# Kernel tuning notes

Measured on AMD Instinct MI355X. Metric: run time of the kernel, lower is better.

Reference implementation:

```python
import jax, jax.numpy as jnp
import numpy as np

N_NODES = 50000
N_EDGES = 800000
D = 128
EPS = 1e-5


def _glorot(key, shape):
    fan_in, fan_out = shape[0], shape[1] if len(shape) > 1 else 1
    s = jnp.sqrt(2.0 / (fan_in + fan_out))
    return jax.random.normal(key, shape, dtype=jnp.float32) * s


def setup_inputs() -> dict:
    key = jax.random.key(0)
    ks = jax.random.split(key, 16)
    h = jax.random.normal(ks[0], (N_NODES, D), dtype=jnp.float32)
    e = jax.random.normal(ks[1], (N_EDGES, D), dtype=jnp.float32)
    src = jax.random.randint(ks[2], (N_EDGES,), 0, N_NODES, dtype=jnp.int32)
    dst = jax.random.randint(ks[3], (N_EDGES,), 0, N_NODES, dtype=jnp.int32)
    # weights stored [in, out] (i.e. torch W.T); biases [out]
    W_fc = _glorot(ks[4], (D, D))
    W_fce = _glorot(ks[5], (D, D))
    a_attn = _glorot(ks[6], (3 * D,))      # attn_fc weight (out=1)
    a_attn_e = _glorot(ks[7], (3 * D,))    # attn_fc_e weight
    W_B1 = _glorot(ks[8], (D, D)); b_B1 = jnp.zeros((D,), jnp.float32)
    W_B2 = _glorot(ks[9], (D, D)); b_B2 = jnp.zeros((D,), jnp.float32)
    W_B3 = _glorot(ks[10], (D, D)); b_B3 = jnp.zeros((D,), jnp.float32)
    W_mix = _glorot(ks[11], (2 * D, D)); b_mix = jnp.zeros((D,), jnp.float32)
    ln_g = jnp.ones((D,), jnp.float32); ln_b = jnp.zeros((D,), jnp.float32)
    return dict(h=h, e=e, src=src, dst=dst, W_fc=W_fc, W_fce=W_fce,
                a_attn=a_attn, a_attn_e=a_attn_e,
                W_B1=W_B1, b_B1=b_B1, W_B2=W_B2, b_B2=b_B2,
                W_B3=W_B3, b_B3=b_B3, W_mix=W_mix, b_mix=b_mix,
                ln_g=ln_g, ln_b=ln_b)


def _segment_softmax(scores, seg, num_segments):
    # scores: [E]; softmax over edges sharing the same destination node
    m = jax.ops.segment_max(scores, seg, num_segments=num_segments)
    ex = jnp.exp(scores - m[seg])
    denom = jax.ops.segment_sum(ex, seg, num_segments=num_segments)
    return ex / denom[seg]


def _gat_side(z, z_e, s, d_idx, a_attn, a_attn_e, W_mix, b_mix, n):
    # attn_fc(concat[z_src, z_e, z_dst]) split into three small matvecs
    d = z.shape[1]
    zs1, zs2, zs3 = z @ a_attn[:d], z_e @ a_attn[d:2 * d], z @ a_attn[2 * d:]
    ze1, ze2, ze3 = z @ a_attn_e[:d], z_e @ a_attn_e[d:2 * d], z @ a_attn_e[2 * d:]
    score = jax.nn.leaky_relu(zs1[s] + zs2 + zs3[d_idx], negative_slope=0.01)
    score_e = jax.nn.leaky_relu(ze1[s] + ze2 + ze3[d_idx], negative_slope=0.01)
    alpha = _segment_softmax(score, d_idx, n)
    alpha_e = _segment_softmax(score_e, d_idx, n)
    h_agg = jax.ops.segment_sum(alpha[:, None] * z[s], d_idx, num_segments=n)
    he_agg = jax.ops.segment_sum(alpha_e[:, None] * z_e, d_idx, num_segments=n)
    return jnp.concatenate([h_agg, he_agg], axis=-1) @ W_mix + b_mix


def reference(h, e, src, dst, W_fc, W_fce, a_attn, a_attn_e,
              W_B1, b_B1, W_B2, b_B2, W_B3, b_B3, W_mix, b_mix, ln_g, ln_b):
    n = h.shape[0]
    B1h = h @ W_B1 + b_B1
    B2h = h @ W_B2 + b_B2
    B3e = e @ W_B3 + b_B3
    # forward-graph edge update: e_ji = relu(B1h[u] + B2h[v] + B3e) + e (residual)
    e_ji = jax.nn.relu(B1h[src] + B2h[dst] + B3e) + e
    z = h @ W_fc
    z_e = e_ji @ W_fce
    # forward graph aggregates into dst; reverse graph into src
    h_f = _gat_side(z, z_e, src, dst, a_attn, a_attn_e, W_mix, b_mix, n)
    h_r = _gat_side(z, z_e, dst, src, a_attn, a_attn_e, W_mix, b_mix, n)
    h_out = h_f + h_r
    # LayerNorm (batch_norm=False branch)
    mu = jnp.mean(h_out, axis=-1, keepdims=True)
    var = jnp.var(h_out, axis=-1, keepdims=True)
    h_out = (h_out - mu) / jnp.sqrt(var + EPS) * ln_g + ln_b
    h_out = jax.nn.relu(h_out) + h  # residual; dropout=0 (eval)
    return h_out, e_ji
```

## Files before the change

### kernel.cpp

```cpp
#include <hip/hip_runtime.h>
#include <hip/hip_bf16.h>


typedef _Float16 f16x8 __attribute__((ext_vector_type(8)));
typedef _Float16 f16x4 __attribute__((ext_vector_type(4)));
typedef _Float16 f16x2 __attribute__((ext_vector_type(2)));
typedef float f32x4 __attribute__((ext_vector_type(4)));

__device__ inline float lrelu(float x) { return x > 0.f ? x : 0.01f * x; }

__device__ inline unsigned short f2bf(float f) {
  unsigned u = __float_as_uint(f);
  unsigned r = (u + 0x7FFFu + ((u >> 16) & 1u)) >> 16;
  return (unsigned short)r;
}
__device__ inline float bf2f(unsigned short us) {
  return __uint_as_float(((unsigned)us) << 16);
}

__global__ void k_combine(const float* __restrict__ Wfc, const float* __restrict__ Wfce,
                          const float* __restrict__ Wmix, const float* __restrict__ aat,
                          const float* __restrict__ aate, _Float16* __restrict__ McT,
                          float* __restrict__ cvec) {
  int b = blockIdx.x, j = threadIdx.x;
  if (b < 256) {
    const float* Arow;
    const float* Wm;
    if (b < 128) { Arow = Wfc + b * 128; Wm = Wmix; }
    else         { Arow = Wfce + (b - 128) * 128; Wm = Wmix + 128 * 128; }
    float acc = 0.f;
    for (int t = 0; t < 128; ++t) acc += Arow[t] * Wm[t * 128 + j];
    McT[j * 256 + b] = (_Float16)acc;
  } else {
    int idx = b - 256;
    const float* W; const float* a;
    switch (idx) {
      case 0: W = Wfc;  a = aat;        break;
      case 1: W = Wfce; a = aat + 128;  break;
      case 2: W = Wfc;  a = aat + 256;  break;
      case 3: W = Wfc;  a = aate;       break;
      case 4: W = Wfce; a = aate + 128; break;
      default: W = Wfc; a = aate + 256; break;
    }
    float acc = 0.f;
    for (int t = 0; t < 128; ++t) acc += W[j * 128 + t] * a[t];
    cvec[idx * 128 + j] = acc;
  }
}

__global__ __launch_bounds__(256) void k_wt3(const float* __restrict__ W3,
                                             const float* __restrict__ W1,
                                             const float* __restrict__ W2,
                                             _Float16* __restrict__ WT,
                                             _Float16* __restrict__ W1T,
                                             _Float16* __restrict__ W2T) {
  int idx = blockIdx.x * 256 + threadIdx.x;
  int which = idx >> 14;
  int r = idx & 16383;
  int c = r >> 7, k = r & 127;
  const float* s = (which == 0) ? W3 : (which == 1) ? W1 : W2;
  _Float16* d = (which == 0) ? WT : (which == 1) ? W1T : W2T;
  d[r] = (_Float16)s[k * 128 + c];
}

__global__ __launch_bounds__(256) void k_gemm_dual(const float* __restrict__ A,
                                                   const _Float16* __restrict__ W1T,
                                                   const float* __restrict__ b1v,
                                                   const _Float16* __restrict__ W2T,
                                                   const float* __restrict__ b2v,
                                                   const float* __restrict__ cvec,
                                                   unsigned short* __restrict__ B1hh,
                                                   unsigned short* __restrict__ B2hh,
                                                   unsigned short* __restrict__ hh,
                                                   float* __restrict__ zs1, float* __restrict__ zs3,
                                                   float* __restrict__ ze1, float* __restrict__ ze3,
                                                   int M) {
  __shared__ float Als[64][132];
  int tid = threadIdx.x;
  int lane = tid & 63, w = tid >> 6;
  int kgrp = lane >> 4, sub = lane & 15;
  long mbase = (long)blockIdx.x * 64;
#pragma unroll
  for (int it = 0; it < 8; ++it) {
    int idx = tid + it * 256;
    int r = idx >> 5, cv = idx & 31;
    long m = mbase + r;
    float4 v = make_float4(0.f, 0.f, 0.f, 0.f);
    if (m < M) v = *(const float4*)&A[m * 128 + 4 * cv];
    *(float4*)&Als[r][4 * cv] = v;
  }
  __syncthreads();

  int arow = w * 16 + sub;
  f16x8 afr[4];
#pragma unroll
  for (int ks = 0; ks < 4; ++ks) {
    float4 u0 = *(const float4*)&Als[arow][ks * 32 + kgrp * 8];
    float4 u1 = *(const float4*)&Als[arow][ks * 32 + kgrp * 8 + 4];
    f16x8 a;
    a[0] = (_Float16)u0.x; a[1] = (_Float16)u0.y; a[2] = (_Float16)u0.z; a[3] = (_Float16)u0.w;
    a[4] = (_Float16)u1.x; a[5] = (_Float16)u1.y; a[6] = (_Float16)u1.z; a[7] = (_Float16)u1.w;
    afr[ks] = a;
  }

  f32x4 acc1[8], acc2[8];
#pragma unroll
  for (int t = 0; t < 8; ++t) {
    acc1[t] = (f32x4){0.f, 0.f, 0.f, 0.f};
    acc2[t] = (f32x4){0.f, 0.f, 0.f, 0.f};
  }
#pragma unroll
  for (int ks = 0; ks < 4; ++ks)
#pragma unroll
    for (int t = 0; t < 8; ++t) {
      int boff = (t * 16 + sub) * 128 + ks * 32 + kgrp * 8;
      f16x8 b1 = *(const f16x8*)&W1T[boff];
      acc1[t] = __builtin_amdgcn_mfma_f32_16x16x32_f16(afr[ks], b1, acc1[t], 0, 0, 0);
      f16x8 b2 = *(const f16x8*)&W2T[boff];
      acc2[t] = __builtin_amdgcn_mfma_f32_16x16x32_f16(afr[ks], b2, acc2[t], 0, 0, 0);
    }

  float bb1[8], bb2[8];
#pragma unroll
  for (int t = 0; t < 8; ++t) {
    int c = t * 16 + sub;
    bb1[t] = b1v[c];
    bb2[t] = b2v[c];
  }

#pragma unroll
  for (int r = 0; r < 4; ++r) {
    int rl = w * 16 + kgrp * 4 + r;
    long m = mbase + rl;
    float p1 = 0.f, p3 = 0.f, q1 = 0.f, q3 = 0.f;
    if (m < M) {
#pragma unroll
      for (int t = 0; t < 8; ++t) {
        int c = t * 16 + sub;
        float a = Als[rl][c];
        B1hh[m * 128 + c] = f2bf(acc1[t][r] + bb1[t]);
        B2hh[m * 128 + c] = f2bf(acc2[t][r] + bb2[t]);
        hh[m * 128 + c] = f2bf(a);
        p1 += a * cvec[c];
        p3 += a * cvec[256 + c];
        q1 += a * cvec[384 + c];
        q3 += a * cvec[640 + c];
      }
    }
#pragma unroll
    for (int mk = 1; mk < 16; mk <<= 1) {
      p1 += __shfl_xor(p1, mk); p3 += __shfl_xor(p3, mk);
      q1 += __shfl_xor(q1, mk); q3 += __shfl_xor(q3, mk);
    }
    if (m < M && sub == 0) { zs1[m] = p1; zs3[m] = p3; ze1[m] = q1; ze3[m] = q3; }
  }
}

__global__ __launch_bounds__(256) void k_edge(const float* __restrict__ e,
                                              const _Float16* __restrict__ WT,
                                              const float* __restrict__ bias,
                                              const unsigned short* __restrict__ B1hh,
                                              const unsigned short* __restrict__ B2hh,
                                              const int* __restrict__ src, const int* __restrict__ dst,
                                              const float* __restrict__ cs2, const float* __restrict__ ce2,
                                              float* __restrict__ eout, unsigned short* __restrict__ ejh,
                                              float* __restrict__ zs2, float* __restrict__ ze2, int M) {
  __shared__ _Float16 Els[64][136];
  int tid = threadIdx.x;
  int lane = tid & 63, w = tid >> 6;
  int kgrp = lane >> 4, sub = lane & 15;
  long mbase = (long)blockIdx.x * 64;
#pragma unroll
  for (int it = 0; it < 8; ++it) {
    int idx = tid + it * 256;
    int r = idx >> 5, cv = idx & 31;
    long m = mbase + r;
    float4 v = make_float4(0.f, 0.f, 0.f, 0.f);
    if (m < M) v = *(const float4*)&e[m * 128 + 4 * cv];
    f16x4 hv;
    hv[0] = (_Float16)v.x; hv[1] = (_Float16)v.y;
    hv[2] = (_Float16)v.z; hv[3] = (_Float16)v.w;
    *(f16x4*)&Els[r][4 * cv] = hv;
  }
  __syncthreads();

  int arow = w * 16 + sub;
  f16x8 afr[4];
#pragma unroll
  for (int ks = 0; ks < 4; ++ks)
    afr[ks] = *(const f16x8*)&Els[arow][ks * 32 + kgrp * 8];

  f32x4 acc[8];
#pragma unroll
  for (int t = 0; t < 8; ++t) acc[t] = (f32x4){0.f, 0.f, 0.f, 0.f};
#pragma unroll
  for (int ks = 0; ks < 4; ++ks)
#pragma unroll
    for (int t = 0; t < 8; ++t) {
      f16x8 b = *(const f16x8*)&WT[(t * 16 + sub) * 128 + ks * 32 + kgrp * 8];
      acc[t] = __builtin_amdgcn_mfma_f32_16x16x32_f16(afr[ks], b, acc[t], 0, 0, 0);
    }

  float bb[8], cs[8], ce[8];
#pragma unroll
  for (int t = 0; t < 8; ++t) {
    int c = t * 16 + sub;
    bb[t] = bias[c];
    cs[t] = cs2[c];
    ce[t] = ce2[c];
  }

#pragma unroll
  for (int r = 0; r < 4; ++r) {
    int rl = w * 16 + kgrp * 4 + r;
    long m = mbase + rl;
    float ps = 0.f, pe = 0.f;
    if (m < M) {
      int s = src[m], dv = dst[m];
      const unsigned short* b1p = B1hh + (long)s * 128;
      const unsigned short* b2p = B2hh + (long)dv * 128;
#pragma unroll
      for (int t = 0; t < 8; ++t) {
        int c = t * 16 + sub;
        float o = fmaxf(acc[t][r] + bb[t] + bf2f(b1p[c]) + bf2f(b2p[c]), 0.f) + (float)Els[rl][c];
        eout[m * 128 + c] = o;
        ejh[m * 128 + c] = f2bf(o);
        ps += o * cs[t];
        pe += o * ce[t];
      }
    }
#pragma unroll
    for (int mk = 1; mk < 16; mk <<= 1) {
      ps += __shfl_xor(ps, mk);
      pe += __shfl_xor(pe, mk);
    }
    if (m < M && sub == 0) { zs2[m] = ps; ze2[m] = pe; }
  }
}

__global__ void k_hist(const int* __restrict__ src, const int* __restrict__ dst,
                       int* __restrict__ cntf, int* __restrict__ cntr, int E) {
  int e = blockIdx.x * 256 + threadIdx.x;
  if (e < E) {
    atomicAdd(&cntf[dst[e]], 1);
    atomicAdd(&cntr[src[e]], 1);
  }
}

__global__ __launch_bounds__(1024) void k_scan(const int* __restrict__ cntf,
                                               const int* __restrict__ cntr,
                                               int* __restrict__ offf, int* __restrict__ offr, int n) {
  __shared__ int part[1024];
  int tid = threadIdx.x;
  for (int pass = 0; pass < 2; ++pass) {
    const int* cnt = pass ? cntr : cntf;
    int* off = pass ? offr : offf;
    int per = (n + 1023) >> 10;
    int beg = tid * per; if (beg > n) beg = n;
    int end = beg + per; if (end > n) end = n;
    int s = 0;
    for (int i = beg; i < end; ++i) s += cnt[i];
    part[tid] = s;
    __syncthreads();
    for (int o = 1; o < 1024; o <<= 1) {
      int vv = (tid >= o) ? part[tid - o] : 0;
      __syncthreads();
      part[tid] += vv;
      __syncthreads();
    }
    int run = tid ? part[tid - 1] : 0;
    for (int i = beg; i < end; ++i) { off[i] = run; run += cnt[i]; }
    if (tid == 1023) off[n] = part[1023];
    __syncthreads();
  }
}

__global__ void k_fill(const int* __restrict__ src, const int* __restrict__ dst,
                       const int* __restrict__ offf, const int* __restrict__ offr,
                       int* __restrict__ curf, int* __restrict__ curr,
                       int* __restrict__ eidf, int* __restrict__ eidr, int E) {
  int e = blockIdx.x * 256 + threadIdx.x;
  if (e >= E) return;
  int d = dst[e];
  int p = atomicAdd(&curf[d], 1);
  eidf[offf[d] + p] = e;
  int s = src[e];
  p = atomicAdd(&curr[s], 1);
  eidr[offr[s] + p] = e;
}

__global__ void k_scores(const int* __restrict__ src, const int* __restrict__ dst,
                         const int* __restrict__ eidf, const int* __restrict__ eidr,
                         const float* __restrict__ zs1, const float* __restrict__ zs2,
                         const float* __restrict__ zs3, const float* __restrict__ ze1,
                         const float* __restrict__ ze2, const float* __restrict__ ze3,
                         float* __restrict__ sf, float* __restrict__ sef,
                         float* __restrict__ sr, float* __restrict__ ser, int E) {
  int p = blockIdx.x * 256 + threadIdx.x;
  if (p >= E) return;
  {
    int e = eidf[p];
    int s = src[e], d = dst[e];
    float z2 = zs2[e], ze2v = ze2[e];
    sf[p] = lrelu(zs1[s] + z2 + zs3[d]);
    sef[p] = lrelu(ze1[s] + ze2v + ze3[d]);
  }
  {
    int e = eidr[p];
    int s = src[e], d = dst[e];
    float z2 = zs2[e], ze2v = ze2[e];
    sr[p] = lrelu(zs1[d] + z2 + zs3[s]);
    ser[p] = lrelu(ze1[d] + ze2v + ze3[s]);
  }
}

__device__ inline float wred_max64(float v) {
#pragma unroll
  for (int mk = 32; mk; mk >>= 1) v = fmaxf(v, __shfl_xor(v, mk));
  return v;
}
__device__ inline float wred_sum64(float v) {
#pragma unroll
  for (int mk = 32; mk; mk >>= 1) v += __shfl_xor(v, mk);
  return v;
}

__global__ __launch_bounds__(256) void k_agg4(const int* __restrict__ offf, const int* __restrict__ eidf,
                                              const int* __restrict__ offr, const int* __restrict__ eidr,
                                              const int* __restrict__ src, const int* __restrict__ dst,
                                              const float* __restrict__ sf, const float* __restrict__ sef,
                                              const float* __restrict__ sr, const float* __restrict__ ser,
                                              const unsigned short* __restrict__ hh,
                                              const unsigned short* __restrict__ ejh,
                                              _Float16* __restrict__ agg2, int n) {
  int gw = blockIdx.x * 4 + (threadIdx.x >> 6);
  int lane = threadIdx.x & 63;
  if (gw >= 2 * n) return;
  int dir = gw & 1;
  int v = gw >> 1;
  const int* off = dir ? offr : offf;
  const int* eid = dir ? eidr : eidf;
  const float* sc  = dir ? sr  : sf;
  const float* sce = dir ? ser : sef;
  const int* nbr = dir ? dst : src;
  int s0 = off[v], s1 = off[v + 1];
  float m1 = -1e30f, m2 = -1e30f;
  for (int i = s0 + lane; i < s1; i += 64) {
    m1 = fmaxf(m1, sc[i]);
    m2 = fmaxf(m2, sce[i]);
  }
  m1 = wred_max64(m1); m2 = wred_max64(m2);
  float d1 = 0.f, d2 = 0.f;
  for (int i = s0 + lane; i < s1; i += 64) {
    d1 += __expf(sc[i] - m1);
    d2 += __expf(sce[i] - m2);
  }
  d1 = wred_sum64(d1); d2 = wred_sum64(d2);
  float i1 = (s1 > s0) ? 1.f / d1 : 0.f;
  float i2 = (s1 > s0) ? 1.f / d2 : 0.f;
  float aH0 = 0.f, aH1 = 0.f, aE0 = 0.f, aE1 = 0.f;
  int i = s0;
  for (; i + 3 < s1; i += 4) {
    int eA = eid[i], eB = eid[i + 1], eC = eid[i + 2], eD = eid[i + 3];
    int nA = nbr[eA], nB = nbr[eB], nC = nbr[eC], nD = nbr[eD];
    unsigned hpA = *(const unsigned*)&hh[(long)nA * 128 + 2 * lane];
    unsigned epA = *(const unsigned*)&ejh[(long)eA * 128 + 2 * lane];
    unsigned hpB = *(const unsigned*)&hh[(long)nB * 128 + 2 * lane];
    unsigned epB = *(const unsigned*)&ejh[(long)eB * 128 + 2 * lane];
    unsigned hpC = *(const unsigned*)&hh[(long)nC * 128 + 2 * lane];
    unsigned epC = *(const unsigned*)&ejh[(long)eC * 128 + 2 * lane];
    unsigned hpD = *(const unsigned*)&hh[(long)nD * 128 + 2 * lane];
    unsigned epD = *(const unsigned*)&ejh[(long)eD * 128 + 2 * lane];
    float w1A = __expf(sc[i] - m1) * i1,     w2A = __expf(sce[i] - m2) * i2;
    float w1B = __expf(sc[i + 1] - m1) * i1, w2B = __expf(sce[i + 1] - m2) * i2;
    float w1C = __expf(sc[i + 2] - m1) * i1, w2C = __expf(sce[i + 2] - m2) * i2;
    float w1D = __expf(sc[i + 3] - m1) * i1, w2D = __expf(sce[i + 3] - m2) * i2;
    aH0 += w1A * bf2f((unsigned short)(hpA & 0xFFFFu)) + w1B * bf2f((unsigned short)(hpB & 0xFFFFu))
         + w1C * bf2f((unsigned short)(hpC & 0xFFFFu)) + w1D * bf2f((unsigned short)(hpD & 0xFFFFu));
    aH1 += w1A * bf2f((unsigned short)(hpA >> 16)) + w1B * bf2f((unsigned short)(hpB >> 16))
         + w1C * bf2f((unsigned short)(hpC >> 16)) + w1D * bf2f((unsigned short)(hpD >> 16));
    aE0 += w2A * bf2f((unsigned short)(epA & 0xFFFFu)) + w2B * bf2f((unsigned short)(epB & 0xFFFFu))
         + w2C * bf2f((unsigned short)(epC & 0xFFFFu)) + w2D * bf2f((unsigned short)(epD & 0xFFFFu));
    aE1 += w2A * bf2f((unsigned short)(epA >> 16)) + w2B * bf2f((unsigned short)(epB >> 16))
         + w2C * bf2f((unsigned short)(epC >> 16)) + w2D * bf2f((unsigned short)(epD >> 16));
  }
  for (; i < s1; ++i) {
    int e_ = eid[i];
    int nb = nbr[e_];
    float w1 = __expf(sc[i] - m1) * i1;
    float w2 = __expf(sce[i] - m2) * i2;
    unsigned hp = *(const unsigned*)&hh[(long)nb * 128 + 2 * lane];
    unsigned ep = *(const unsigned*)&ejh[(long)e_ * 128 + 2 * lane];
    aH0 += w1 * bf2f((unsigned short)(hp & 0xFFFFu));
    aH1 += w1 * bf2f((unsigned short)(hp >> 16));
    aE0 += w2 * bf2f((unsigned short)(ep & 0xFFFFu));
    aE1 += w2 * bf2f((unsigned short)(ep >> 16));
  }
  _Float16* dstp = agg2 + ((long)dir * n + v) * 256;
  *(f16x2*)&dstp[2 * lane] = (f16x2){(_Float16)aH0, (_Float16)aH1};
  *(f16x2*)&dstp[128 + 2 * lane] = (f16x2){(_Float16)aE0, (_Float16)aE1};
}

__global__ __launch_bounds__(256) void k_mix_ln(const _Float16* __restrict__ A,
                                                const _Float16* __restrict__ McT,
                                                const float* __restrict__ bias,
                                                const float* __restrict__ h,
                                                const float* __restrict__ g,
                                                const float* __restrict__ bn,
                                                float* __restrict__ outp, int M) {
  __shared__ _Float16 Als[64][264];
  int tid = threadIdx.x;
  int lane = tid & 63, w = tid >> 6;
  int kgrp = lane >> 4, sub = lane & 15;
  long mbase = (long)blockIdx.x * 64;
  const _Float16* A2 = A + (long)M * 256;
#pragma unroll
  for (int it = 0; it < 8; ++it) {
    int idx = tid + it * 256;
    int r = idx >> 5, c8 = (idx & 31) * 8;
    long m = mbase + r;
    f16x8 hv = (f16x8){0, 0, 0, 0, 0, 0, 0, 0};
    if (m < M) {
      f16x8 v1 = *(const f16x8*)&A[m * 256 + c8];
      f16x8 v2 = *(const f16x8*)&A2[m * 256 + c8];
#pragma unroll
      for (int j = 0; j < 8; ++j) hv[j] = (_Float16)((float)v1[j] + (float)v2[j]);
    }
    *(f16x8*)&Als[r][c8] = hv;
  }
  __syncthreads();

  int arow = w * 16 + sub;
  f32x4 acc[8];
#pragma unroll
  for (int t = 0; t < 8; ++t) acc[t] = (f32x4){0.f, 0.f, 0.f, 0.f};
#pragma unroll
  for (int ks = 0; ks < 8; ++ks) {
    f16x8 a = *(const f16x8*)&Als[arow][ks * 32 + kgrp * 8];
#pragma unroll
    for (int t = 0; t < 8; ++t) {
      f16x8 b = *(const f16x8*)&McT[(t * 16 + sub) * 256 + ks * 32 + kgrp * 8];
      acc[t] = __builtin_amdgcn_mfma_f32_16x16x32_f16(a, b, acc[t], 0, 0, 0);
    }
  }

  float bb[8], gv[8], bv[8];
#pragma unroll
  for (int t = 0; t < 8; ++t) {
    int c = t * 16 + sub;
    bb[t] = 2.f * bias[c];
    gv[t] = g[c];
    bv[t] = bn[c];
  }

#pragma unroll
  for (int r = 0; r < 4; ++r) {
    int rl = w * 16 + kgrp * 4 + r;
    long m = mbase + rl;
    float x[8];
    float s = 0.f, q = 0.f;
#pragma unroll
    for (int t = 0; t < 8; ++t) {
      x[t] = acc[t][r] + bb[t];
      s += x[t];
      q += x[t] * x[t];
    }
#pragma unroll
    for (int mk = 1; mk < 16; mk <<= 1) {
      s += __shfl_xor(s, mk);
      q += __shfl_xor(q, mk);
    }
    float mu = s * (1.f / 128.f);
    float var = q * (1.f / 128.f) - mu * mu;
    float rstd = rsqrtf(var + 1e-5f);
    if (m < M) {
      const float* hp = h + m * 128;
#pragma unroll
      for (int t = 0; t < 8; ++t) {
        int c = t * 16 + sub;
        outp[m * 128 + c] = fmaxf((x[t] - mu) * rstd * gv[t] + bv[t], 0.f) + hp[c];
      }
    }
  }
}

extern "C" void kernel_launch(void* const* d_in, const int* in_sizes, int n_in,
                              void* d_out, int out_size, void* d_ws, size_t ws_size,
                              hipStream_t stream) {
  const float* h = (const float*)d_in[0];
  const float* e = (const float*)d_in[1];
  const int* src = (const int*)d_in[2];
  const int* dst = (const int*)d_in[3];
  const float* Wfc = (const float*)d_in[4];
  const float* Wfce = (const float*)d_in[5];
  const float* aat = (const float*)d_in[6];
  const float* aate = (const float*)d_in[7];
  const float* WB1 = (const float*)d_in[8];
  const float* bB1 = (const float*)d_in[9];
  const float* WB2 = (const float*)d_in[10];
  const float* bB2 = (const float*)d_in[11];
  const float* WB3 = (const float*)d_in[12];
  const float* bB3 = (const float*)d_in[13];
  const float* Wmix = (const float*)d_in[14];
  const float* bmix = (const float*)d_in[15];
  const float* lng = (const float*)d_in[16];
  const float* lnb = (const float*)d_in[17];
  int n = in_sizes[0] / 128;
  int E = in_sizes[1] / 128;

  float* hout = (float*)d_out;
  float* eout = (float*)d_out + (size_t)n * 128;

  char* w = (char*)d_ws;
  auto alloc = [&](size_t bytes) {
    void* p = w;
    w += (bytes + 255) / 256 * 256;
    return p;
  };
  unsigned short* B1hh = (unsigned short*)alloc((size_t)n * 128 * 2);
  unsigned short* B2hh = (unsigned short*)alloc((size_t)n * 128 * 2);
  _Float16* agg2 = (_Float16*)alloc((size_t)n * 512 * 2);
  float* zs1 = (float*)alloc((size_t)n * 4);
  float* zs3 = (float*)alloc((size_t)n * 4);
  float* ze1 = (float*)alloc((size_t)n * 4);
  float* ze3 = (float*)alloc((size_t)n * 4);
  float* zs2 = (float*)alloc((size_t)E * 4);
  float* ze2 = (float*)alloc((size_t)E * 4);
  float* sf = (float*)alloc((size_t)E * 4);
  float* sef = (float*)alloc((size_t)E * 4);
  float* sr = (float*)alloc((size_t)E * 4);
  float* ser = (float*)alloc((size_t)E * 4);
  float* cvec = (float*)alloc(768 * 4);
  _Float16* WT = (_Float16*)alloc(128 * 128 * 2);
  _Float16* W1T = (_Float16*)alloc(128 * 128 * 2);
  _Float16* W2T = (_Float16*)alloc(128 * 128 * 2);
  _Float16* McT = (_Float16*)alloc(128 * 256 * 2);
  int* offf = (int*)alloc((size_t)(n + 1) * 4);
  int* offr = (int*)alloc((size_t)(n + 1) * 4);
  size_t curpad = ((size_t)n * 4 + 255) / 256 * 256;
  int* curf = (int*)alloc((size_t)n * 4);
  int* curr = (int*)alloc((size_t)n * 4);
  int* eidf = (int*)alloc((size_t)E * 4);
  int* eidr = (int*)alloc((size_t)E * 4);
  unsigned short* ejh = (unsigned short*)alloc((size_t)E * 128 * 2);
  unsigned short* hh = (unsigned short*)alloc((size_t)n * 128 * 2);

  hipMemsetAsync(curf, 0, curpad * 2, stream);

  k_combine<<<262, 128, 0, stream>>>(Wfc, Wfce, Wmix, aat, aate, McT, cvec);
  k_wt3<<<192, 256, 0, stream>>>(WB3, WB1, WB2, WT, W1T, W2T);
  k_gemm_dual<<<(n + 63) / 64, 256, 0, stream>>>(h, W1T, bB1, W2T, bB2, cvec, B1hh, B2hh, hh,
                                                 zs1, zs3, ze1, ze3, n);
  k_hist<<<(E + 255) / 256, 256, 0, stream>>>(src, dst, curf, curr, E);
  k_scan<<<1, 1024, 0, stream>>>(curf, curr, offf, offr, n);
  hipMemsetAsync(curf, 0, curpad * 2, stream);
  k_fill<<<(E + 255) / 256, 256, 0, stream>>>(src, dst, offf, offr, curf, curr, eidf, eidr, E);
  k_edge<<<(E + 63) / 64, 256, 0, stream>>>(e, WT, bB3, B1hh, B2hh, src, dst,
                                            cvec + 128, cvec + 512, eout, ejh, zs2, ze2, E);
  k_scores<<<(E + 255) / 256, 256, 0, stream>>>(src, dst, eidf, eidr, zs1, zs2, zs3, ze1, ze2, ze3,
                                                sf, sef, sr, ser, E);
  k_agg4<<<(2 * n + 3) / 4, 256, 0, stream>>>(offf, eidf, offr, eidr, src, dst, sf, sef, sr, ser,
                                              hh, ejh, agg2, n);
  k_mix_ln<<<(n + 63) / 64, 256, 0, stream>>>(agg2, McT, bmix, h, lng, lnb, hout, n);
}
```

Baseline: 1.080 ms.

## Store bf16 edge features in forward-CSR order and precompute neighbor indices

k_edge now writes the bf16 copy of e_ji at each edge's forward-CSR position (posf), so the forward aggregation reads edge rows contiguously instead of gathering them through eidf. k_scores also materialises per-slot neighbor ids (nf, nr) and reverse-direction row positions (er2), which removes the double-indirection eid->src/dst lookups from k_agg4. The cost is scattered bf16 writes in k_edge, extra index arrays and writes in k_fill and k_scores, and a branch in k_agg4 that duplicates its loop per direction.

```diff
diff --git a/kernel.cpp b/kernel.cpp
--- a/kernel.cpp
+++ b/kernel.cpp
@@ -162,6 +162,7 @@
                                               const unsigned short* __restrict__ B1hh,
                                               const unsigned short* __restrict__ B2hh,
                                               const int* __restrict__ src, const int* __restrict__ dst,
+                                              const int* __restrict__ posf,
                                               const float* __restrict__ cs2, const float* __restrict__ ce2,
                                               float* __restrict__ eout, unsigned short* __restrict__ ejh,
                                               float* __restrict__ zs2, float* __restrict__ ze2, int M) {
@@ -217,6 +218,7 @@
     float ps = 0.f, pe = 0.f;
     if (m < M) {
       int s = src[m], dv = dst[m];
+      long pf = posf[m];
       const unsigned short* b1p = B1hh + (long)s * 128;
       const unsigned short* b2p = B2hh + (long)dv * 128;
 #pragma unroll
@@ -224,7 +226,7 @@
         int c = t * 16 + sub;
         float o = fmaxf(acc[t][r] + bb[t] + bf2f(b1p[c]) + bf2f(b2p[c]), 0.f) + (float)Els[rl][c];
         eout[m * 128 + c] = o;
-        ejh[m * 128 + c] = f2bf(o);
+        ejh[pf * 128 + c] = f2bf(o);
         ps += o * cs[t];
         pe += o * ce[t];
       }
@@ -278,12 +280,15 @@
 __global__ void k_fill(const int* __restrict__ src, const int* __restrict__ dst,
                        const int* __restrict__ offf, const int* __restrict__ offr,
                        int* __restrict__ curf, int* __restrict__ curr,
-                       int* __restrict__ eidf, int* __restrict__ eidr, int E) {
+                       int* __restrict__ eidf, int* __restrict__ eidr,
+                       int* __restrict__ posf, int* E_unused, int E) {
   int e = blockIdx.x * 256 + threadIdx.x;
   if (e >= E) return;
   int d = dst[e];
   int p = atomicAdd(&curf[d], 1);
-  eidf[offf[d] + p] = e;
+  int qf = offf[d] + p;
+  eidf[qf] = e;
+  posf[e] = qf;
   int s = src[e];
   p = atomicAdd(&curr[s], 1);
   eidr[offr[s] + p] = e;
@@ -291,11 +296,14 @@
 
 __global__ void k_scores(const int* __restrict__ src, const int* __restrict__ dst,
                          const int* __restrict__ eidf, const int* __restrict__ eidr,
+                         const int* __restrict__ posf,
                          const float* __restrict__ zs1, const float* __restrict__ zs2,
                          const float* __restrict__ zs3, const float* __restrict__ ze1,
                          const float* __restrict__ ze2, const float* __restrict__ ze3,
                          float* __restrict__ sf, float* __restrict__ sef,
-                         float* __restrict__ sr, float* __restrict__ ser, int E) {
+                         float* __restrict__ sr, float* __restrict__ ser,
+                         int* __restrict__ nf, int* __restrict__ nr,
+                         int* __restrict__ er2, int E) {
   int p = blockIdx.x * 256 + threadIdx.x;
   if (p >= E) return;
   {
@@ -304,6 +312,7 @@
     float z2 = zs2[e], ze2v = ze2[e];
     sf[p] = lrelu(zs1[s] + z2 + zs3[d]);
     sef[p] = lrelu(ze1[s] + ze2v + ze3[d]);
+    nf[p] = s;
   }
   {
     int e = eidr[p];
@@ -311,6 +320,8 @@
     float z2 = zs2[e], ze2v = ze2[e];
     sr[p] = lrelu(zs1[d] + z2 + zs3[s]);
     ser[p] = lrelu(ze1[d] + ze2v + ze3[s]);
+    nr[p] = d;
+    er2[p] = posf[e];
   }
 }
 
@@ -325,9 +336,10 @@
   return v;
 }
 
-__global__ __launch_bounds__(256) void k_agg4(const int* __restrict__ offf, const int* __restrict__ eidf,
-                                              const int* __restrict__ offr, const int* __restrict__ eidr,
-                                              const int* __restrict__ src, const int* __restrict__ dst,
+__global__ __launch_bounds__(256) void k_agg4(const int* __restrict__ offf,
+                                              const int* __restrict__ offr,
+                                              const int* __restrict__ nf, const int* __restrict__ nr,
+                                              const int* __restrict__ er2,
                                               const float* __restrict__ sf, const float* __restrict__ sef,
                                               const float* __restrict__ sr, const float* __restrict__ ser,
                                               const unsigned short* __restrict__ hh,
@@ -339,10 +351,9 @@
   int dir = gw & 1;
   int v = gw >> 1;
   const int* off = dir ? offr : offf;
-  const int* eid = dir ? eidr : eidf;
   const float* sc  = dir ? sr  : sf;
   const float* sce = dir ? ser : sef;
-  const int* nbr = dir ? dst : src;
+  const int* nbArr = dir ? nr : nf;
   int s0 = off[v], s1 = off[v + 1];
   float m1 = -1e30f, m2 = -1e30f;
   for (int i = s0 + lane; i < s1; i += 64) {
@@ -360,41 +371,78 @@
   float i2 = (s1 > s0) ? 1.f / d2 : 0.f;
   float aH0 = 0.f, aH1 = 0.f, aE0 = 0.f, aE1 = 0.f;
   int i = s0;
-  for (; i + 3 < s1; i += 4) {
-    int eA = eid[i], eB = eid[i + 1], eC = eid[i + 2], eD = eid[i + 3];
-    int nA = nbr[eA], nB = nbr[eB], nC = nbr[eC], nD = nbr[eD];
-    unsigned hpA = *(const unsigned*)&hh[(long)nA * 128 + 2 * lane];
-    unsigned epA = *(const unsigned*)&ejh[(long)eA * 128 + 2 * lane];
-    unsigned hpB = *(const unsigned*)&hh[(long)nB * 128 + 2 * lane];
-    unsigned epB = *(const unsigned*)&ejh[(long)eB * 128 + 2 * lane];
-    unsigned hpC = *(const unsigned*)&hh[(long)nC * 128 + 2 * lane];
-    unsigned epC = *(const unsigned*)&ejh[(long)eC * 128 + 2 * lane];
-    unsigned hpD = *(const unsigned*)&hh[(long)nD * 128 + 2 * lane];
-    unsigned epD = *(const unsigned*)&ejh[(long)eD * 128 + 2 * lane];
-    float w1A = __expf(sc[i] - m1) * i1,     w2A = __expf(sce[i] - m2) * i2;
-    float w1B = __expf(sc[i + 1] - m1) * i1, w2B = __expf(sce[i + 1] - m2) * i2;
-    float w1C = __expf(sc[i + 2] - m1) * i1, w2C = __expf(sce[i + 2] - m2) * i2;
-    float w1D = __expf(sc[i + 3] - m1) * i1, w2D = __expf(sce[i + 3] - m2) * i2;
-    aH0 += w1A * bf2f((unsigned short)(hpA & 0xFFFFu)) + w1B * bf2f((unsigned short)(hpB & 0xFFFFu))
-         + w1C * bf2f((unsigned short)(hpC & 0xFFFFu)) + w1D * bf2f((unsigned short)(hpD & 0xFFFFu));
-    aH1 += w1A * bf2f((unsigned short)(hpA >> 16)) + w1B * bf2f((unsigned short)(hpB >> 16))
-         + w1C * bf2f((unsigned short)(hpC >> 16)) + w1D * bf2f((unsigned short)(hpD >> 16));
-    aE0 += w2A * bf2f((unsigned short)(epA & 0xFFFFu)) + w2B * bf2f((unsigned short)(epB & 0xFFFFu))
-         + w2C * bf2f((unsigned short)(epC & 0xFFFFu)) + w2D * bf2f((unsigned short)(epD & 0xFFFFu));
-    aE1 += w2A * bf2f((unsigned short)(epA >> 16)) + w2B * bf2f((unsigned short)(epB >> 16))
-         + w2C * bf2f((unsigned short)(epC >> 16)) + w2D * bf2f((unsigned short)(epD >> 16));
-  }
-  for (; i < s1; ++i) {
-    int e_ = eid[i];
-    int nb = nbr[e_];
-    float w1 = __expf(sc[i] - m1) * i1;
-    float w2 = __expf(sce[i] - m2) * i2;
-    unsigned hp = *(const unsigned*)&hh[(long)nb * 128 + 2 * lane];
-    unsigned ep = *(const unsigned*)&ejh[(long)e_ * 128 + 2 * lane];
-    aH0 += w1 * bf2f((unsigned short)(hp & 0xFFFFu));
-    aH1 += w1 * bf2f((unsigned short)(hp >> 16));
-    aE0 += w2 * bf2f((unsigned short)(ep & 0xFFFFu));
-    aE1 += w2 * bf2f((unsigned short)(ep >> 16));
+  if (dir == 0) {
+    for (; i + 3 < s1; i += 4) {
+      int nA = nf[i], nB = nf[i + 1], nC = nf[i + 2], nD = nf[i + 3];
+      unsigned hpA = *(const unsigned*)&hh[(long)nA * 128 + 2 * lane];
+      unsigned epA = *(const unsigned*)&ejh[(long)i * 128 + 2 * lane];
+      unsigned hpB = *(const unsigned*)&hh[(long)nB * 128 + 2 * lane];
+      unsigned epB = *(const unsigned*)&ejh[(long)(i + 1) * 128 + 2 * lane];
+      unsigned hpC = *(const unsigned*)&hh[(long)nC * 128 + 2 * lane];
+      unsigned epC = *(const unsigned*)&ejh[(long)(i + 2) * 128 + 2 * lane];
+      unsigned hpD = *(const unsigned*)&hh[(long)nD * 128 + 2 * lane];
+      unsigned epD = *(const unsigned*)&ejh[(long)(i + 3) * 128 + 2 * lane];
+      float w1A = __expf(sc[i] - m1) * i1,     w2A = __expf(sce[i] - m2) * i2;
+      float w1B = __expf(sc[i + 1] - m1) * i1, w2B = __expf(sce[i + 1] - m2) * i2;
+      float w1C = __expf(sc[i + 2] - m1) * i1, w2C = __expf(sce[i + 2] - m2) * i2;
+      float w1D = __expf(sc[i + 3] - m1) * i1, w2D = __expf(sce[i + 3] - m2) * i2;
+      aH0 += w1A * bf2f((unsigned short)(hpA & 0xFFFFu)) + w1B * bf2f((unsigned short)(hpB & 0xFFFFu))
+           + w1C * bf2f((unsigned short)(hpC & 0xFFFFu)) + w1D * bf2f((unsigned short)(hpD & 0xFFFFu));
+      aH1 += w1A * bf2f((unsigned short)(hpA >> 16)) + w1B * bf2f((unsigned short)(hpB >> 16))
+           + w1C * bf2f((unsigned short)(hpC >> 16)) + w1D * bf2f((unsigned short)(hpD >> 16));
+      aE0 += w2A * bf2f((unsigned short)(epA & 0xFFFFu)) + w2B * bf2f((unsigned short)(epB & 0xFFFFu))
+           + w2C * bf2f((unsigned short)(epC & 0xFFFFu)) + w2D * bf2f((unsigned short)(epD & 0xFFFFu));
+      aE1 += w2A * bf2f((unsigned short)(epA >> 16)) + w2B * bf2f((unsigned short)(epB >> 16))
+           + w2C * bf2f((unsigned short)(epC >> 16)) + w2D * bf2f((unsigned short)(epD >> 16));
+    }
+    for (; i < s1; ++i) {
+      int nb = nf[i];
+      float w1 = __expf(sc[i] - m1) * i1;
+      float w2 = __expf(sce[i] - m2) * i2;
+      unsigned hp = *(const unsigned*)&hh[(long)nb * 128 + 2 * lane];
+      unsigned ep = *(const unsigned*)&ejh[(long)i * 128 + 2 * lane];
+      aH0 += w1 * bf2f((unsigned short)(hp & 0xFFFFu));
+      aH1 += w1 * bf2f((unsigned short)(hp >> 16));
+      aE0 += w2 * bf2f((unsigned short)(ep & 0xFFFFu));
+      aE1 += w2 * bf2f((unsigned short)(ep >> 16));
+    }
+  } else {
+    for (; i + 3 < s1; i += 4) {
+      int nA = nr[i], nB = nr[i + 1], nC = nr[i + 2], nD = nr[i + 3];
+      int rA = er2[i], rB = er2[i + 1], rC = er2[i + 2], rD = er2[i + 3];
+      unsigned hpA = *(const unsigned*)&hh[(long)nA * 128 + 2 * lane];
+      unsigned epA = *(const unsigned*)&ejh[(long)rA * 128 + 2 * lane];
+      unsigned hpB = *(const unsigned*)&hh[(long)nB * 128 + 2 * lane];
+      unsigned epB = *(const unsigned*)&ejh[(long)rB * 128 + 2 * lane];
+      unsigned hpC = *(const unsigned*)&hh[(long)nC * 128 + 2 * lane];
+      unsigned epC = *(const unsigned*)&ejh[(long)rC * 128 + 2 * lane];
+      unsigned hpD = *(const unsigned*)&hh[(long)nD * 128 + 2 * lane];
+      unsigned epD = *(const unsigned*)&ejh[(long)rD * 128 + 2 * lane];
+      float w1A = __expf(sc[i] - m1) * i1,     w2A = __expf(sce[i] - m2) * i2;
+      float w1B = __expf(sc[i + 1] - m1) * i1, w2B = __expf(sce[i + 1] - m2) * i2;
+      float w1C = __expf(sc[i + 2] - m1) * i1, w2C = __expf(sce[i + 2] - m2) * i2;
+      float w1D = __expf(sc[i + 3] - m1) * i1, w2D = __expf(sce[i + 3] - m2) * i2;
+      aH0 += w1A * bf2f((unsigned short)(hpA & 0xFFFFu)) + w1B * bf2f((unsigned short)(hpB & 0xFFFFu))
+           + w1C * bf2f((unsigned short)(hpC & 0xFFFFu)) + w1D * bf2f((unsigned short)(hpD & 0xFFFFu));
+      aH1 += w1A * bf2f((unsigned short)(hpA >> 16)) + w1B * bf2f((unsigned short)(hpB >> 16))
+           + w1C * bf2f((unsigned short)(hpC >> 16)) + w1D * bf2f((unsigned short)(hpD >> 16));
+      aE0 += w2A * bf2f((unsigned short)(epA & 0xFFFFu)) + w2B * bf2f((unsigned short)(epB & 0xFFFFu))
+           + w2C * bf2f((unsigned short)(epC & 0xFFFFu)) + w2D * bf2f((unsigned short)(epD & 0xFFFFu));
+      aE1 += w2A * bf2f((unsigned short)(epA >> 16)) + w2B * bf2f((unsigned short)(epB >> 16))
+           + w2C * bf2f((unsigned short)(epC >> 16)) + w2D * bf2f((unsigned short)(epD >> 16));
+    }
+    for (; i < s1; ++i) {
+      int nb = nr[i];
+      int rr_ = er2[i];
+      float w1 = __expf(sc[i] - m1) * i1;
+      float w2 = __expf(sce[i] - m2) * i2;
+      unsigned hp = *(const unsigned*)&hh[(long)nb * 128 + 2 * lane];
+      unsigned ep = *(const unsigned*)&ejh[(long)rr_ * 128 + 2 * lane];
+      aH0 += w1 * bf2f((unsigned short)(hp & 0xFFFFu));
+      aH1 += w1 * bf2f((unsigned short)(hp >> 16));
+      aE0 += w2 * bf2f((unsigned short)(ep & 0xFFFFu));
+      aE1 += w2 * bf2f((unsigned short)(ep >> 16));
+    }
   }
   _Float16* dstp = agg2 + ((long)dir * n + v) * 256;
   *(f16x2*)&dstp[2 * lane] = (f16x2){(_Float16)aH0, (_Float16)aH1};
@@ -542,6 +590,10 @@
   int* curr = (int*)alloc((size_t)n * 4);
   int* eidf = (int*)alloc((size_t)E * 4);
   int* eidr = (int*)alloc((size_t)E * 4);
+  int* posf = (int*)alloc((size_t)E * 4);
+  int* nf = (int*)alloc((size_t)E * 4);
+  int* nr = (int*)alloc((size_t)E * 4);
+  int* er2 = (int*)alloc((size_t)E * 4);
   unsigned short* ejh = (unsigned short*)alloc((size_t)E * 128 * 2);
   unsigned short* hh = (unsigned short*)alloc((size_t)n * 128 * 2);
 
@@ -554,12 +606,13 @@
   k_hist<<<(E + 255) / 256, 256, 0, stream>>>(src, dst, curf, curr, E);
   k_scan<<<1, 1024, 0, stream>>>(curf, curr, offf, offr, n);
   hipMemsetAsync(curf, 0, curpad * 2, stream);
-  k_fill<<<(E + 255) / 256, 256, 0, stream>>>(src, dst, offf, offr, curf, curr, eidf, eidr, E);
-  k_edge<<<(E + 63) / 64, 256, 0, stream>>>(e, WT, bB3, B1hh, B2hh, src, dst,
+  k_fill<<<(E + 255) / 256, 256, 0, stream>>>(src, dst, offf, offr, curf, curr, eidf, eidr,
+                                              posf, nullptr, E);
+  k_edge<<<(E + 63) / 64, 256, 0, stream>>>(e, WT, bB3, B1hh, B2hh, src, dst, posf,
                                             cvec + 128, cvec + 512, eout, ejh, zs2, ze2, E);
-  k_scores<<<(E + 255) / 256, 256, 0, stream>>>(src, dst, eidf, eidr, zs1, zs2, zs3, ze1, ze2, ze3,
-                                                sf, sef, sr, ser, E);
-  k_agg4<<<(2 * n + 3) / 4, 256, 0, stream>>>(offf, eidf, offr, eidr, src, dst, sf, sef, sr, ser,
+  k_scores<<<(E + 255) / 256, 256, 0, stream>>>(src, dst, eidf, eidr, posf, zs1, zs2, zs3,
+                                                ze1, ze2, ze3, sf, sef, sr, ser, nf, nr, er2, E);
+  k_agg4<<<(2 * n + 3) / 4, 256, 0, stream>>>(offf, offr, nf, nr, er2, sf, sef, sr, ser,
                                               hh, ejh, agg2, n);
   k_mix_ln<<<(n + 63) / 64, 256, 0, stream>>>(agg2, McT, bmix, h, lng, lnb, hout, n);
 }
```

Result: faster. 1.045 ms (-3.2%).
